# Kernel tuning notes

Hardware: AMD Instinct MI355X
Metric: run time of the kernel (lower is better)

Reference implementation:

```python
import jax, jax.numpy as jnp
import numpy as np

B, N, S, D, H = 4, 64, 512, 128, 8  # batch, groups, set size, in_size, heads


def setup_inputs() -> dict:
    key = jax.random.key(0)
    ks = jax.random.split(key, 8)
    s1 = 1.0 / np.sqrt(D)
    s2 = 1.0 / np.sqrt(2 * D)
    return {
        "x": jax.random.normal(ks[0], (B, N, S, D), jnp.float32),
        # DeepSets phi MLP: D -> D -> D -> D (hidden=[in_size,in_size])
        "w1": jax.random.normal(ks[1], (D, D), jnp.float32) * s1,
        "b1": jnp.zeros((D,), jnp.float32),
        "w2": jax.random.normal(ks[2], (D, D), jnp.float32) * s1,
        "b2": jnp.zeros((D,), jnp.float32),
        "w3": jax.random.normal(ks[3], (D, D), jnp.float32) * s1,
        "b3": jnp.zeros((D,), jnp.float32),
        # attention projection: 2D -> H*D
        "W": jax.random.normal(ks[4], (2 * D, H * D), jnp.float32) * s2,
        "Wb": jnp.zeros((H * D,), jnp.float32),
        # per-head query vector (zeros-init in original; random for a nontrivial baseline)
        "q": jax.random.normal(ks[5], (H, D), jnp.float32) * 0.1,
    }


def reference(x, w1, b1, w2, b2, w3, b3, W, Wb, q):
    # SetTransform (DeepSets): per-element MLP then sum over set dim (-2)
    h = jax.nn.relu(x @ w1 + b1)
    h = jax.nn.relu(h @ w2 + b2)
    h = h @ w3 + b3
    set_feat = h.sum(axis=-2)                                  # (B, N, D)
    sf = jnp.broadcast_to(set_feat[..., None, :], x.shape)      # (B, N, S, D)
    comb = jnp.concatenate([x, sf], axis=-1)                    # (B, N, S, 2D)
    heads = (comb @ W + Wb).reshape(B, N, S, H, D)              # (B, N, S, H, D)
    e = jnp.einsum('bnshd,hd->bnsh', heads, q)                  # (B, N, S, H)
    return jax.nn.softmax(e, axis=-2)                           # softmax over set dim
```

## Files before the change

kernel.cpp:

```cpp
#include <hip/hip_runtime.h>

#define Bsz 4
#define Ngrp 64
#define Sset 512
#define Din 128
#define Hh 8
#define EST (Sset + 1)

__global__ void __launch_bounds__(Din) compute_u_kernel(
    const float* __restrict__ W,
    const float* __restrict__ q,
    float* __restrict__ u)
{
    const int h = blockIdx.x;
    const int d = threadIdx.x;

    __shared__ float qs[Din];
    qs[d] = q[h * Din + d];
    __syncthreads();

    const float4* Wr = (const float4*)(W + (size_t)d * (Hh * Din) + (size_t)h * Din);
    const float4* q4 = (const float4*)qs;

    float acc = 0.f;
#pragma unroll
    for (int j = 0; j < Din / 4; ++j) {
        float4 wv = Wr[j];
        float4 qv = q4[j];
        acc = fmaf(wv.x, qv.x, acc);
        acc = fmaf(wv.y, qv.y, acc);
        acc = fmaf(wv.z, qv.z, acc);
        acc = fmaf(wv.w, qv.w, acc);
    }
    u[h * Din + d] = acc;
}

__global__ void __launch_bounds__(Sset) attn_softmax_kernel(
    const float* __restrict__ x,
    const float* __restrict__ u,
    float* __restrict__ out)
{
    const int bn = blockIdx.x;
    const int tid = threadIdx.x;

    __shared__ float e_s[Hh * EST];

    {
        const int s = tid;
        const float4* xr = (const float4*)(x + ((size_t)bn * Sset + s) * Din);
        const float4* u4 = (const float4*)u;

        float acc[Hh];
#pragma unroll
        for (int h = 0; h < Hh; ++h) acc[h] = 0.f;

#pragma unroll 4
        for (int j = 0; j < Din / 4; ++j) {
            float4 xv = xr[j];
#pragma unroll
            for (int h = 0; h < Hh; ++h) {
                float4 wv = u4[h * (Din / 4) + j];
                acc[h] = fmaf(xv.x, wv.x, acc[h]);
                acc[h] = fmaf(xv.y, wv.y, acc[h]);
                acc[h] = fmaf(xv.z, wv.z, acc[h]);
                acc[h] = fmaf(xv.w, wv.w, acc[h]);
            }
        }
#pragma unroll
        for (int h = 0; h < Hh; ++h) e_s[h * EST + s] = acc[h];
    }
    __syncthreads();

    {
        const int w = tid >> 6;
        const int lane = tid & 63;
        float* eh = &e_s[w * EST];

        float m = -1e30f;
#pragma unroll
        for (int k = 0; k < Sset / 64; ++k) m = fmaxf(m, eh[lane + 64 * k]);
#pragma unroll
        for (int off = 32; off >= 1; off >>= 1) m = fmaxf(m, __shfl_xor(m, off, 64));

        float p[Sset / 64];
        float sum = 0.f;
#pragma unroll
        for (int k = 0; k < Sset / 64; ++k) {
            p[k] = __expf(eh[lane + 64 * k] - m);
            sum += p[k];
        }
#pragma unroll
        for (int off = 32; off >= 1; off >>= 1) sum += __shfl_xor(sum, off, 64);

        const float inv = 1.f / sum;
#pragma unroll
        for (int k = 0; k < Sset / 64; ++k) eh[lane + 64 * k] = p[k] * inv;
    }
    __syncthreads();

    {
        const int s = tid;
        float4 o0, o1;
        o0.x = e_s[0 * EST + s];
        o0.y = e_s[1 * EST + s];
        o0.z = e_s[2 * EST + s];
        o0.w = e_s[3 * EST + s];
        o1.x = e_s[4 * EST + s];
        o1.y = e_s[5 * EST + s];
        o1.z = e_s[6 * EST + s];
        o1.w = e_s[7 * EST + s];
        float4* orow = (float4*)(out + ((size_t)bn * Sset + s) * Hh);
        orow[0] = o0;
        orow[1] = o1;
    }
}

extern "C" void kernel_launch(void* const* d_in, const int* in_sizes, int n_in,
                              void* d_out, int out_size, void* d_ws, size_t ws_size,
                              hipStream_t stream) {
    const float* x = (const float*)d_in[0];
    const float* W = (const float*)d_in[7];
    const float* q = (const float*)d_in[9];
    float* u = (float*)d_ws;
    float* out = (float*)d_out;

    compute_u_kernel<<<dim3(Hh), dim3(Din), 0, stream>>>(W, q, u);
    attn_softmax_kernel<<<dim3(Bsz * Ngrp), dim3(Sset), 0, stream>>>(x, u, out);
}
```

Before: 123.9 us.

## Coalesce x loads with 16-lane row groups and shuffle reductions

The projection phase of the attention kernel now assigns 16 lanes to each set row, so each row's x is read with contiguous float4 loads across lanes instead of one thread striding through a whole row. The per-head u vectors are held in registers, and dot products are finished with xor-shuffle reductions. This targets uncoalesced global reads of x, which is the dominant memory traffic. In exchange it adds four shuffles per head per row and more register pressure.

Result: no change. 125.4 us (+1.2%).

```diff
diff --git a/kernel.cpp b/kernel.cpp
--- a/kernel.cpp
+++ b/kernel.cpp
@@ -13,13 +13,13 @@
     float* __restrict__ u)
 {
     const int h = blockIdx.x;
-    const int d = threadIdx.x;
+    const int c = threadIdx.x;
 
     __shared__ float qs[Din];
-    qs[d] = q[h * Din + d];
+    qs[c] = q[h * Din + c];
     __syncthreads();
 
-    const float4* Wr = (const float4*)(W + (size_t)d * (Hh * Din) + (size_t)h * Din);
+    const float4* Wr = (const float4*)(W + (size_t)c * (Hh * Din) + (size_t)h * Din);
     const float4* q4 = (const float4*)qs;
 
     float acc = 0.f;
@@ -32,7 +32,7 @@
         acc = fmaf(wv.z, qv.z, acc);
         acc = fmaf(wv.w, qv.w, acc);
     }
-    u[h * Din + d] = acc;
+    u[h * Din + c] = acc;
 }
 
 __global__ void __launch_bounds__(Sset) attn_softmax_kernel(
@@ -42,39 +42,53 @@
 {
     const int bn = blockIdx.x;
     const int tid = threadIdx.x;
+    const int wave = tid >> 6;
+    const int lane = tid & 63;
+    const int g    = lane >> 4;
+    const int sub  = lane & 15;
 
     __shared__ float e_s[Hh * EST];
 
-    {
-        const int s = tid;
-        const float4* xr = (const float4*)(x + ((size_t)bn * Sset + s) * Din);
-        const float4* u4 = (const float4*)u;
+    const float4* u4 = (const float4*)u;
+    float4 ua[Hh], ub[Hh];
+#pragma unroll
+    for (int h = 0; h < Hh; ++h) {
+        ua[h] = u4[h * 32 + sub];
+        ub[h] = u4[h * 32 + sub + 16];
+    }
 
-        float acc[Hh];
+    const float4* xb = (const float4*)(x + (size_t)bn * Sset * Din);
+#pragma unroll 4
+    for (int pass = 0; pass < 16; ++pass) {
+        const int r = wave * 64 + pass * 4 + g;
+        const float4* xr = xb + (size_t)r * (Din / 4);
+        const float4 x0 = xr[sub];
+        const float4 x1 = xr[sub + 16];
+
+        float st = 0.f;
 #pragma unroll
-        for (int h = 0; h < Hh; ++h) acc[h] = 0.f;
-
-#pragma unroll 4
-        for (int j = 0; j < Din / 4; ++j) {
-            float4 xv = xr[j];
-#pragma unroll
-            for (int h = 0; h < Hh; ++h) {
-                float4 wv = u4[h * (Din / 4) + j];
-                acc[h] = fmaf(xv.x, wv.x, acc[h]);
-                acc[h] = fmaf(xv.y, wv.y, acc[h]);
-                acc[h] = fmaf(xv.z, wv.z, acc[h]);
-                acc[h] = fmaf(xv.w, wv.w, acc[h]);
-            }
+        for (int h = 0; h < Hh; ++h) {
+            float v;
+            v = x0.x * ua[h].x;
+            v = fmaf(x0.y, ua[h].y, v);
+            v = fmaf(x0.z, ua[h].z, v);
+            v = fmaf(x0.w, ua[h].w, v);
+            v = fmaf(x1.x, ub[h].x, v);
+            v = fmaf(x1.y, ub[h].y, v);
+            v = fmaf(x1.z, ub[h].z, v);
+            v = fmaf(x1.w, ub[h].w, v);
+            v += __shfl_xor(v, 1);
+            v += __shfl_xor(v, 2);
+            v += __shfl_xor(v, 4);
+            v += __shfl_xor(v, 8);
+            if (sub == h) st = v;
         }
-#pragma unroll
-        for (int h = 0; h < Hh; ++h) e_s[h * EST + s] = acc[h];
+        if (sub < Hh) e_s[sub * EST + r] = st;
     }
     __syncthreads();
 
     {
-        const int w = tid >> 6;
-        const int lane = tid & 63;
-        float* eh = &e_s[w * EST];
+        float* eh = &e_s[wave * EST];
 
         float m = -1e30f;
 #pragma unroll
```
